# Kernel optimization log

Measured on AMD Instinct MI355X. Metric: run time of the kernel, lower is better.

Reference implementation:

```python
import jax, jax.numpy as jnp
import numpy as np

B, S, D = 2, 2048, 1024
H, DH = 16, 64  # num_head, head_dim; H*DH == D


def setup_inputs() -> dict:
    key = jax.random.key(0)
    ks = jax.random.split(key, 10)
    stdv = 1.0 / np.sqrt(D)
    def lin(k):
        kw, kb = jax.random.split(k)
        W = jax.random.uniform(kw, (D, D), jnp.float32, -stdv, stdv)
        b = jax.random.uniform(kb, (D,), jnp.float32, -stdv, stdv)
        return W, b
    Wq, bq = lin(ks[0]); Wk, bk = lin(ks[1]); Wv, bv = lin(ks[2]); Wo, bo = lin(ks[3])
    x = jax.random.normal(ks[4], (B, S, D), jnp.float32)
    # causal mask: True = attend
    mask = jnp.tril(jnp.ones((S, S), jnp.bool_))
    mask = jnp.broadcast_to(mask, (B, S, S))
    return {"x": x, "mask": mask, "Wq": Wq, "bq": bq, "Wk": Wk, "bk": bk,
            "Wv": Wv, "bv": bv, "Wo": Wo, "bo": bo}


def _split_head(t):
    # [B,S,D] -> [B*H, S, DH]
    return t.reshape(B, S, H, DH).transpose(0, 2, 1, 3).reshape(B * H, S, DH)


def _concat_head(t):
    # [B*H, S, DH] -> [B, S, D]
    return t.reshape(B, H, S, DH).transpose(0, 2, 1, 3).reshape(B, S, D)


def reference(x, mask, Wq, bq, Wk, bk, Wv, bv, Wo, bo):
    q = _split_head(x @ Wq.T + bq)
    k = _split_head(x @ Wk.T + bk)
    v = _split_head(x @ Wv.T + bv)
    scale = 1.0 / jnp.sqrt(jnp.float32(DH))
    # scores: [B, H, S, S], masked softmax (flash-attention math, unfused ref)
    scores = jnp.einsum('nqd,nkd->nqk', q, k).reshape(B, H, S, S) * scale
    scores = jnp.where(mask[:, None, :, :], scores, jnp.finfo(scores.dtype).min)
    attn = jax.nn.softmax(scores, axis=-1)
    out = jnp.einsum('bhqk,nkd->bhqd', attn, v.reshape(B, H, S, DH).reshape(B * H, S, DH)).reshape(B * H, S, DH) if False else jnp.einsum('nqk,nkd->nqd', attn.reshape(B * H, S, S), v)
    return _concat_head(out) @ Wo.T + bo
```

## Files before the change

### kernel.cpp

```cpp
#include <hip/hip_runtime.h>
#include <cstdint>

#define S_LEN  2048
#define NH     16
#define DHEAD  64
#define DMODEL 1024

typedef __bf16 bf16x8 __attribute__((ext_vector_type(8)));
typedef __bf16 bf16x2 __attribute__((ext_vector_type(2)));
typedef float  f32x4  __attribute__((ext_vector_type(4)));

__device__ __forceinline__ unsigned short f2bf(float x) {
  union { float f; unsigned int u; } c; c.f = x;
  unsigned int u = c.u;
  return (unsigned short)((u + 0x7fffu + ((u >> 16) & 1u)) >> 16);
}

__device__ __forceinline__ unsigned int pkbf(float a, float b) {
#if __has_builtin(__builtin_amdgcn_cvt_pk_bf16_f32)
  bf16x2 r = __builtin_amdgcn_cvt_pk_bf16_f32(a, b);
  return *(unsigned int*)&r;
#else
  return (unsigned int)f2bf(a) | ((unsigned int)f2bf(b) << 16);
#endif
}

__device__ __forceinline__ unsigned short f2bf1(float x) {
#if __has_builtin(__builtin_amdgcn_cvt_pk_bf16_f32)
  bf16x2 r = __builtin_amdgcn_cvt_pk_bf16_f32(x, x);
  union { bf16x2 v; unsigned int u; } c; c.v = r;
  return (unsigned short)(c.u & 0xffffu);
#else
  return f2bf(x);
#endif
}

__device__ __forceinline__ __bf16 us2bf(unsigned short u) {
  union { unsigned short u; __bf16 b; } c; c.u = u; return c.b;
}

__device__ __forceinline__ void glds16(const void* g, void* l) {
  __builtin_amdgcn_global_load_lds(
      (const __attribute__((address_space(1))) void*)g,
      (__attribute__((address_space(3))) void*)l, 16, 0, 0);
}

__device__ __forceinline__ f32x4 mfma16(bf16x8 a, bf16x8 b, f32x4 c) {
  return __builtin_amdgcn_mfma_f32_16x16x32_bf16(a, b, c, 0, 0, 0);
}

__global__ void cvt_all(const float* __restrict__ x,
                        const float* __restrict__ Wq,
                        const float* __restrict__ Wk,
                        const float* __restrict__ Wv,
                        const float* __restrict__ Wo,
                        unsigned short* __restrict__ xb,
                        unsigned short* __restrict__ wqkv,
                        unsigned short* __restrict__ wo) {
  const int b = blockIdx.x;
  const float* src;
  unsigned short* dst;
  int off;
  if (b < 4096)      { src = x;  dst = xb;                off = b; }
  else if (b < 5120) { src = Wq; dst = wqkv;              off = b - 4096; }
  else if (b < 6144) { src = Wk; dst = wqkv + (1 << 20);  off = b - 5120; }
  else if (b < 7168) { src = Wv; dst = wqkv + (2 << 20);  off = b - 6144; }
  else               { src = Wo; dst = wo;                off = b - 7168; }
  const int i = (off * 256 + threadIdx.x) * 4;
  float4 v = *(const float4*)&src[i];
  uint2 r;
  r.x = pkbf(v.x, v.y);
  r.y = pkbf(v.z, v.w);
  *(uint2*)&dst[i] = r;
}

template<int MODE, int BN>
__global__ __launch_bounds__(256)
void gemm_bt(const unsigned short* __restrict__ A,
             const unsigned short* __restrict__ W,
             const float* __restrict__ bias0,
             const float* __restrict__ bias1,
             const float* __restrict__ bias2,
             unsigned short* __restrict__ Qt,
             unsigned short* __restrict__ Kb,
             unsigned short* __restrict__ Vt,
             float* __restrict__ Out,
             int K) {
  constexpr int JN = BN / 32;
  __shared__ __align__(16) unsigned short As[2][128 * 32];
  __shared__ __align__(16) unsigned short Bs[2][BN * 32];
  const int t    = threadIdx.x;
  const int lane = t & 63;
  const int w    = t >> 6;
  const int lr   = lane & 15, lq = lane >> 4;
  const int wm   = (w >> 1) * 64, wn = (w & 1) * (BN / 2);
  const int m0   = blockIdx.y * 128, n0 = blockIdx.x * BN;
  const int ra   = t >> 2, ca = (t & 3) * 8;

  f32x4 acc[4][JN] = {};

  const int niter = K >> 6;
  for (int kk = 0; kk < niter; ++kk) {
    const int k0 = kk << 6;
#pragma unroll
    for (int kh = 0; kh < 2; ++kh) {
      const int kc = k0 + kh * 32;
      glds16(A + (m0 + ra) * K + kc + ca,      &As[kh][ra * 32 + ca]);
      glds16(A + (m0 + 64 + ra) * K + kc + ca, &As[kh][(64 + ra) * 32 + ca]);
      glds16(W + (n0 + ra) * K + kc + ca,      &Bs[kh][ra * 32 + ca]);
      if (BN == 128)
        glds16(W + (n0 + 64 + ra) * K + kc + ca, &Bs[kh][(64 + ra) * 32 + ca]);
    }
    __syncthreads();
#pragma unroll
    for (int kh = 0; kh < 2; ++kh) {
      bf16x8 af[4], bg[JN];
#pragma unroll
      for (int i = 0; i < 4; ++i)
        af[i] = *(const bf16x8*)&As[kh][(wm + i * 16 + lr) * 32 + lq * 8];
#pragma unroll
      for (int j = 0; j < JN; ++j)
        bg[j] = *(const bf16x8*)&Bs[kh][(wn + j * 16 + lr) * 32 + lq * 8];
#pragma unroll
      for (int i = 0; i < 4; ++i)
#pragma unroll
        for (int j = 0; j < JN; ++j)
          acc[i][j] = mfma16(af[i], bg[j], acc[i][j]);
    }
    __syncthreads();
  }

  if (MODE == 0) {
    const int tsel = n0 >> 10;
#pragma unroll
    for (int i = 0; i < 4; ++i) {
#pragma unroll
      for (int j = 0; j < JN; ++j) {
        const int mb = m0 + wm + i * 16 + lq * 4;
        const int n  = n0 + wn + j * 16 + lr;
        const int d  = n & 1023;
        const int bidx = mb >> 11, s = mb & (S_LEN - 1);
        const int h = d >> 6, dh = d & 63;
        const int bh = bidx * NH + h;
        const float bv0 = (tsel == 0) ? bias0[d] : ((tsel == 1) ? bias1[d] : bias2[d]);
        if (tsel == 0) {
          const float sc = 0.125f * 1.44269504088896f;
          uint2 pv;
          pv.x = pkbf((acc[i][j][0] + bv0) * sc, (acc[i][j][1] + bv0) * sc);
          pv.y = pkbf((acc[i][j][2] + bv0) * sc, (acc[i][j][3] + bv0) * sc);
          *(uint2*)&Qt[(bh * DHEAD + dh) * S_LEN + s] = pv;
        } else if (tsel == 2) {
          uint2 pv;
          pv.x = pkbf(acc[i][j][0] + bv0, acc[i][j][1] + bv0);
          pv.y = pkbf(acc[i][j][2] + bv0, acc[i][j][3] + bv0);
          *(uint2*)&Vt[(bh * DHEAD + dh) * S_LEN + s] = pv;
        } else {
#pragma unroll
          for (int r = 0; r < 4; ++r)
            Kb[(bh * S_LEN + s + r) * DHEAD + dh] = f2bf1(acc[i][j][r] + bv0);
        }
      }
    }
  } else {
#pragma unroll
    for (int i = 0; i < 4; ++i)
#pragma unroll
      for (int j = 0; j < JN; ++j)
#pragma unroll
        for (int r = 0; r < 4; ++r) {
          const int m = m0 + wm + i * 16 + lq * 4 + r;
          const int n = n0 + wn + j * 16 + lr;
          Out[m * DMODEL + n] = acc[i][j][r] + bias0[n];
        }
  }
}

__global__ __launch_bounds__(256, 2)
void flash_kernel(const unsigned short* __restrict__ Qt,
                  const unsigned short* __restrict__ Kb,
                  const unsigned short* __restrict__ Vt,
                  unsigned short* __restrict__ Ocat) {
  __shared__ __align__(16) unsigned short Ks[2][2][64 * 32];
  __shared__ __align__(16) unsigned short Vs[2][2][64 * 32];
  __shared__ __align__(16) unsigned short pls[4][1024];
  const int w = threadIdx.x >> 6, lane = threadIdx.x & 63;
  const int lr = lane & 15, lq = lane >> 4;
  const int bh = blockIdx.x;
  const int pp = blockIdx.y;
  const char* Kc = (const char*)(Kb + bh * (S_LEN * DHEAD));
  const char* Vc = (const char*)(Vt + bh * (DHEAD * S_LEN));
  const unsigned short* Qp = Qt + bh * (DHEAD * S_LEN);
  const int bb = bh >> 4, h = bh & 15;
  unsigned short* pw = &pls[w][0];
  const int swz = lr & 7;

  const int hh  = w & 1;
  const int rbb = (w >> 1) * 2;
  const int rlane = lane >> 2;
  const int slane = lane & 3;
  const int swslot = (slane ^ ((rlane >> 1) & 3)) * 16;
  const int rsw = (lq ^ ((lr >> 1) & 3)) * 8;

  bf16x8 ones;
#pragma unroll
  for (int j = 0; j < 8; ++j) ones[j] = (__bf16)1.0f;

  auto run_strip = [&](int sb) {
    const int nfull = sb;
    const int q0 = sb * 64 + w * 16;
    bf16x8 qlo, qhi;
#pragma unroll
    for (int j = 0; j < 8; ++j) {
      qlo[j] = us2bf(Qp[(lq * 8 + j) * S_LEN + q0 + lr]);
      qhi[j] = us2bf(Qp[(32 + lq * 8 + j) * S_LEN + q0 + lr]);
    }
    f32x4 o[4] = {};
    f32x4 lacc = {};

    auto stage = [&](int buf, int kt) {
      const int sk0 = kt << 6;
#pragma unroll
      for (int j = 0; j < 2; ++j) {
        const int rb = rbb + j;
        glds16(Kc + (sk0 + rb * 16 + rlane) * 128 + hh * 64 + swslot,
               &Ks[buf][hh][rb * 16 * 32]);
        glds16(Vc + (rb * 16 + rlane) * 4096 + (sk0 + hh * 32) * 2 + swslot,
               &Vs[buf][hh][rb * 16 * 32]);
      }
    };

    stage(0, 0);
    for (int kt = 0; kt <= nfull; ++kt) {
      const int buf = kt & 1;
      __syncthreads();
      if (kt < nfull) stage(1 - buf, kt + 1);

      f32x4 st[4] = {};
      const unsigned short* Kl = Ks[buf][0];
      const unsigned short* Kh = Ks[buf][1];
#pragma unroll
      for (int t = 0; t < 4; ++t) {
        st[t] = mfma16(*(const bf16x8*)&Kl[(t * 16 + lr) * 32 + rsw], qlo, st[t]);
        st[t] = mfma16(*(const bf16x8*)&Kh[(t * 16 + lr) * 32 + rsw], qhi, st[t]);
      }
      float p[4][4];
#pragma unroll
      for (int t = 0; t < 4; ++t)
#pragma unroll
        for (int r = 0; r < 4; ++r)
          p[t][r] = __builtin_amdgcn_exp2f(st[t][r]);
      if (kt == nfull) {
        const int q = q0 + lr, sk0 = kt << 6;
#pragma unroll
        for (int t = 0; t < 4; ++t)
#pragma unroll
          for (int r = 0; r < 4; ++r) {
            const int k = sk0 + t * 16 + lq * 4 + r;
            if (k > q) p[t][r] = 0.f;
          }
      }

#pragma unroll
      for (int t = 0; t < 4; ++t) {
        uint2 pk;
        pk.x = pkbf(p[t][0], p[t][1]);
        pk.y = pkbf(p[t][2], p[t][3]);
        const int g = t * 2 + (lq >> 1);
        *(uint2*)&pw[lr * 64 + ((g ^ swz) << 3) + ((lq & 1) << 2)] = pk;
      }
      const bf16x8 pf0 = *(const bf16x8*)&pw[lr * 64 + ((lq ^ swz) << 3)];
      const bf16x8 pf1 = *(const bf16x8*)&pw[lr * 64 + (((4 + lq) ^ swz) << 3)];
      const unsigned short* Vl = Vs[buf][0];
      const unsigned short* Vh = Vs[buf][1];
#pragma unroll
      for (int tt = 0; tt < 4; ++tt) {
        o[tt] = mfma16(*(const bf16x8*)&Vl[(tt * 16 + lr) * 32 + rsw], pf0, o[tt]);
        o[tt] = mfma16(*(const bf16x8*)&Vh[(tt * 16 + lr) * 32 + rsw], pf1, o[tt]);
      }
      lacc = mfma16(ones, pf0, lacc);
      lacc = mfma16(ones, pf1, lacc);
    }

    const float inv = 1.f / lacc[0];
#pragma unroll
    for (int tt = 0; tt < 4; ++tt) {
      uint2 ov;
      ov.x = pkbf(o[tt][0] * inv, o[tt][1] * inv);
      ov.y = pkbf(o[tt][2] * inv, o[tt][3] * inv);
      *(uint2*)&Ocat[(bb * S_LEN + q0 + lr) * DMODEL + h * DHEAD + tt * 16 + lq * 4] = ov;
    }
    __syncthreads();
  };

  run_strip(31 - pp);
  run_strip(pp);
}

extern "C" void kernel_launch(void* const* d_in, const int* in_sizes, int n_in,
                              void* d_out, int out_size, void* d_ws, size_t ws_size,
                              hipStream_t stream) {
  const float* x  = (const float*)d_in[0];
  const float* Wq = (const float*)d_in[2];
  const float* bq = (const float*)d_in[3];
  const float* Wk = (const float*)d_in[4];
  const float* bk = (const float*)d_in[5];
  const float* Wv = (const float*)d_in[6];
  const float* bv = (const float*)d_in[7];
  const float* Wo = (const float*)d_in[8];
  const float* bo = (const float*)d_in[9];
  float* out = (float*)d_out;

  char* ws = (char*)d_ws;
  unsigned short* xb   = (unsigned short*)(ws);
  unsigned short* wqkv = (unsigned short*)(ws + (8ull  << 20));
  unsigned short* wo   = (unsigned short*)(ws + (14ull << 20));
  unsigned short* Qt   = (unsigned short*)(ws + (16ull << 20));
  unsigned short* Kb   = (unsigned short*)(ws + (24ull << 20));
  unsigned short* Vt   = (unsigned short*)(ws + (32ull << 20));
  unsigned short* Ocat = (unsigned short*)(ws + (40ull << 20));

  cvt_all<<<8192, 256, 0, stream>>>(x, Wq, Wk, Wv, Wo, xb, wqkv, wo);

  gemm_bt<0, 128><<<dim3(24, 32), 256, 0, stream>>>(xb, wqkv, bq, bk, bv,
                                                    Qt, Kb, Vt, nullptr, 1024);
  flash_kernel<<<dim3(32, 16), 256, 0, stream>>>(Qt, Kb, Vt, Ocat);
  gemm_bt<1, 64><<<dim3(16, 32), 256, 0, stream>>>(Ocat, wo, bo, nullptr, nullptr,
                                                   nullptr, nullptr, nullptr, out, 1024);
}
```

Measured before the change: 201.4 us.

## Rewrite flash attention with 32x32 MFMA, split-K waves and permlane P reuse

Moves the flash kernel from 16x16x32 to 32x32x16 bf16 MFMA. Each wave now owns 32 query rows and handles alternate 64-key tiles, so two waves split the key range and their partial O and row sums are merged through LDS at the end. The P operand is rearranged with permlane32_swap instead of a round trip through LDS, and Q is now stored row-major so each lane loads it as a vector. This adds swizzled 64-wide K/V staging, an LDS reduction step and more registers per wave, which may lower occupancy.

```diff
diff --git a/kernel.cpp b/kernel.cpp
--- a/kernel.cpp
+++ b/kernel.cpp
@@ -9,6 +9,7 @@
 typedef __bf16 bf16x8 __attribute__((ext_vector_type(8)));
 typedef __bf16 bf16x2 __attribute__((ext_vector_type(2)));
 typedef float  f32x4  __attribute__((ext_vector_type(4)));
+typedef float  f32x16 __attribute__((ext_vector_type(16)));
 
 __device__ __forceinline__ unsigned short f2bf(float x) {
   union { float f; unsigned int u; } c; c.f = x;
@@ -47,6 +48,20 @@
 
 __device__ __forceinline__ f32x4 mfma16(bf16x8 a, bf16x8 b, f32x4 c) {
   return __builtin_amdgcn_mfma_f32_16x16x32_bf16(a, b, c, 0, 0, 0);
+}
+
+__device__ __forceinline__ f32x16 mfma32(bf16x8 a, bf16x8 b, f32x16 c) {
+  return __builtin_amdgcn_mfma_f32_32x32x16_bf16(a, b, c, 0, 0, 0);
+}
+
+__device__ __forceinline__ void plswap(unsigned int &a, unsigned int &b) {
+#if __has_builtin(__builtin_amdgcn_permlane32_swap)
+  typedef unsigned int uint2v __attribute__((ext_vector_type(2)));
+  uint2v r = __builtin_amdgcn_permlane32_swap(a, b, false, false);
+  a = r[0]; b = r[1];
+#else
+  asm("v_permlane32_swap_b32 %0, %1" : "+v"(a), "+v"(b));
+#endif
 }
 
 __global__ void cvt_all(const float* __restrict__ x,
@@ -145,10 +160,9 @@
         const float bv0 = (tsel == 0) ? bias0[d] : ((tsel == 1) ? bias1[d] : bias2[d]);
         if (tsel == 0) {
           const float sc = 0.125f * 1.44269504088896f;
-          uint2 pv;
-          pv.x = pkbf((acc[i][j][0] + bv0) * sc, (acc[i][j][1] + bv0) * sc);
-          pv.y = pkbf((acc[i][j][2] + bv0) * sc, (acc[i][j][3] + bv0) * sc);
-          *(uint2*)&Qt[(bh * DHEAD + dh) * S_LEN + s] = pv;
+#pragma unroll
+          for (int r = 0; r < 4; ++r)
+            Qt[(bh * S_LEN + s + r) * DHEAD + dh] = f2bf1((acc[i][j][r] + bv0) * sc);
         } else if (tsel == 2) {
           uint2 pv;
           pv.x = pkbf(acc[i][j][0] + bv0, acc[i][j][1] + bv0);
@@ -180,114 +194,139 @@
                   const unsigned short* __restrict__ Kb,
                   const unsigned short* __restrict__ Vt,
                   unsigned short* __restrict__ Ocat) {
-  __shared__ __align__(16) unsigned short Ks[2][2][64 * 32];
-  __shared__ __align__(16) unsigned short Vs[2][2][64 * 32];
-  __shared__ __align__(16) unsigned short pls[4][1024];
+  __shared__ __align__(16) unsigned short Ks[2][2][64 * 64];
+  __shared__ __align__(16) unsigned short Vs[2][2][64 * 64];
+  __shared__ float MlS[2][32];
   const int w = threadIdx.x >> 6, lane = threadIdx.x & 63;
-  const int lr = lane & 15, lq = lane >> 4;
+  const int l31 = lane & 31, half = lane >> 5;
+  const int qh = w & 1, sub = w >> 1;
   const int bh = blockIdx.x;
   const int pp = blockIdx.y;
   const char* Kc = (const char*)(Kb + bh * (S_LEN * DHEAD));
   const char* Vc = (const char*)(Vt + bh * (DHEAD * S_LEN));
-  const unsigned short* Qp = Qt + bh * (DHEAD * S_LEN);
-  const int bb = bh >> 4, h = bh & 15;
-  unsigned short* pw = &pls[w][0];
-  const int swz = lr & 7;
-
-  const int hh  = w & 1;
-  const int rbb = (w >> 1) * 2;
-  const int rlane = lane >> 2;
-  const int slane = lane & 3;
-  const int swslot = (slane ^ ((rlane >> 1) & 3)) * 16;
-  const int rsw = (lq ^ ((lr >> 1) & 3)) * 8;
+  const unsigned short* Qp = Qt + bh * (S_LEN * DHEAD);
+  const int bb = bh >> 4, hd = bh & 15;
 
   bf16x8 ones;
 #pragma unroll
   for (int j = 0; j < 8; ++j) ones[j] = (__bf16)1.0f;
 
   auto run_strip = [&](int sb) {
-    const int nfull = sb;
-    const int q0 = sb * 64 + w * 16;
-    bf16x8 qlo, qhi;
-#pragma unroll
-    for (int j = 0; j < 8; ++j) {
-      qlo[j] = us2bf(Qp[(lq * 8 + j) * S_LEN + q0 + lr]);
-      qhi[j] = us2bf(Qp[(32 + lq * 8 + j) * S_LEN + q0 + lr]);
-    }
-    f32x4 o[4] = {};
-    f32x4 lacc = {};
-
-    auto stage = [&](int buf, int kt) {
-      const int sk0 = kt << 6;
-#pragma unroll
-      for (int j = 0; j < 2; ++j) {
-        const int rb = rbb + j;
-        glds16(Kc + (sk0 + rb * 16 + rlane) * 128 + hh * 64 + swslot,
-               &Ks[buf][hh][rb * 16 * 32]);
-        glds16(Vc + (rb * 16 + rlane) * 4096 + (sk0 + hh * 32) * 2 + swslot,
-               &Vs[buf][hh][rb * 16 * 32]);
+    const int len = sb + 1;
+    const int nit = (len + 1) >> 1;
+    const int q0 = sb * 64;
+    const int qa = q0 + qh * 32 + l31;
+    bf16x8 qf[4];
+#pragma unroll
+    for (int d = 0; d < 4; ++d)
+      qf[d] = *(const bf16x8*)&Qp[qa * 64 + d * 16 + half * 8];
+    f32x16 o0 = {}, o1 = {}, lacc = {};
+
+    auto stage = [&](int buf, int it) {
+#pragma unroll
+      for (int s2 = 0; s2 < 2; ++s2) {
+        const int kt = 2 * it + s2;
+#pragma unroll
+        for (int h8 = 0; h8 < 2; ++h8) {
+          const int rb = w * 16 + h8 * 8;
+          const int r  = rb + (lane >> 3);
+          const int gs = (lane & 7) ^ (r & 7) ^ ((r >> 3) & 3);
+          glds16(Kc + (kt * 64 + r) * 128 + gs * 16, &Ks[buf][s2][rb * 64]);
+          glds16(Vc + r * 4096 + kt * 128 + gs * 16, &Vs[buf][s2][rb * 64]);
+        }
       }
     };
 
     stage(0, 0);
-    for (int kt = 0; kt <= nfull; ++kt) {
-      const int buf = kt & 1;
+    for (int it = 0; it < nit; ++it) {
+      const int buf = it & 1;
       __syncthreads();
-      if (kt < nfull) stage(1 - buf, kt + 1);
-
-      f32x4 st[4] = {};
-      const unsigned short* Kl = Ks[buf][0];
-      const unsigned short* Kh = Ks[buf][1];
-#pragma unroll
-      for (int t = 0; t < 4; ++t) {
-        st[t] = mfma16(*(const bf16x8*)&Kl[(t * 16 + lr) * 32 + rsw], qlo, st[t]);
-        st[t] = mfma16(*(const bf16x8*)&Kh[(t * 16 + lr) * 32 + rsw], qhi, st[t]);
-      }
-      float p[4][4];
-#pragma unroll
-      for (int t = 0; t < 4; ++t)
-#pragma unroll
-        for (int r = 0; r < 4; ++r)
-          p[t][r] = __builtin_amdgcn_exp2f(st[t][r]);
-      if (kt == nfull) {
-        const int q = q0 + lr, sk0 = kt << 6;
-#pragma unroll
-        for (int t = 0; t < 4; ++t)
-#pragma unroll
-          for (int r = 0; r < 4; ++r) {
-            const int k = sk0 + t * 16 + lq * 4 + r;
-            if (k > q) p[t][r] = 0.f;
+      if (it + 1 < nit) stage(1 - buf, it + 1);
+      const int kt = 2 * it + sub;
+      if (kt < len) {
+        const unsigned short* Kt = &Ks[buf][sub][0];
+        const unsigned short* Vl = &Vs[buf][sub][0];
+        const int r0 = l31, r1 = 32 + l31;
+        const int x0 = (r0 & 7) ^ ((r0 >> 3) & 3);
+        const int x1 = (r1 & 7) ^ ((r1 >> 3) & 3);
+        f32x16 st0 = {}, st1 = {};
+#pragma unroll
+        for (int d = 0; d < 4; ++d) {
+          const int sl = d * 2 + half;
+          st0 = mfma32(*(const bf16x8*)&Kt[r0 * 64 + ((sl ^ x0) << 3)], qf[d], st0);
+          st1 = mfma32(*(const bf16x8*)&Kt[r1 * 64 + ((sl ^ x1) << 3)], qf[d], st1);
+        }
+        const bool diag = (kt == sb);
+        unsigned int pk0[8], pk1[8];
+#pragma unroll
+        for (int m = 0; m < 8; ++m) {
+          const int rA = 2 * m, rB = 2 * m + 1;
+          const int kA = (rA & 3) + 8 * (rA >> 2) + 4 * half;
+          const int kB = (rB & 3) + 8 * (rB >> 2) + 4 * half;
+          float e0 = __builtin_amdgcn_exp2f(st0[rA]);
+          float e1 = __builtin_amdgcn_exp2f(st0[rB]);
+          float f0 = __builtin_amdgcn_exp2f(st1[rA]);
+          float f1 = __builtin_amdgcn_exp2f(st1[rB]);
+          if (diag) {
+            e0 = (kt * 64 + kA > qa) ? 0.f : e0;
+            e1 = (kt * 64 + kB > qa) ? 0.f : e1;
+            f0 = (kt * 64 + 32 + kA > qa) ? 0.f : f0;
+            f1 = (kt * 64 + 32 + kB > qa) ? 0.f : f1;
           }
-      }
-
-#pragma unroll
-      for (int t = 0; t < 4; ++t) {
-        uint2 pk;
-        pk.x = pkbf(p[t][0], p[t][1]);
-        pk.y = pkbf(p[t][2], p[t][3]);
-        const int g = t * 2 + (lq >> 1);
-        *(uint2*)&pw[lr * 64 + ((g ^ swz) << 3) + ((lq & 1) << 2)] = pk;
-      }
-      const bf16x8 pf0 = *(const bf16x8*)&pw[lr * 64 + ((lq ^ swz) << 3)];
-      const bf16x8 pf1 = *(const bf16x8*)&pw[lr * 64 + (((4 + lq) ^ swz) << 3)];
-      const unsigned short* Vl = Vs[buf][0];
-      const unsigned short* Vh = Vs[buf][1];
-#pragma unroll
-      for (int tt = 0; tt < 4; ++tt) {
-        o[tt] = mfma16(*(const bf16x8*)&Vl[(tt * 16 + lr) * 32 + rsw], pf0, o[tt]);
-        o[tt] = mfma16(*(const bf16x8*)&Vh[(tt * 16 + lr) * 32 + rsw], pf1, o[tt]);
-      }
-      lacc = mfma16(ones, pf0, lacc);
-      lacc = mfma16(ones, pf1, lacc);
-    }
-
-    const float inv = 1.f / lacc[0];
-#pragma unroll
-    for (int tt = 0; tt < 4; ++tt) {
-      uint2 ov;
-      ov.x = pkbf(o[tt][0] * inv, o[tt][1] * inv);
-      ov.y = pkbf(o[tt][2] * inv, o[tt][3] * inv);
-      *(uint2*)&Ocat[(bb * S_LEN + q0 + lr) * DMODEL + h * DHEAD + tt * 16 + lq * 4] = ov;
+          pk0[m] = pkbf(e0, e1);
+          pk1[m] = pkbf(f0, f1);
+        }
+#pragma unroll
+        for (int s = 0; s < 4; ++s) {
+          unsigned int u, u2, v, v2;
+          if (s == 0)      { u = pk0[0]; u2 = pk0[1]; v = pk0[2]; v2 = pk0[3]; }
+          else if (s == 1) { u = pk0[4]; u2 = pk0[5]; v = pk0[6]; v2 = pk0[7]; }
+          else if (s == 2) { u = pk1[0]; u2 = pk1[1]; v = pk1[2]; v2 = pk1[3]; }
+          else             { u = pk1[4]; u2 = pk1[5]; v = pk1[6]; v2 = pk1[7]; }
+          plswap(u, v);
+          plswap(u2, v2);
+          union { unsigned int ui[4]; bf16x8 bv; } pf;
+          pf.ui[0] = u; pf.ui[1] = u2; pf.ui[2] = v; pf.ui[3] = v2;
+          const int sl = s * 2 + half;
+          o0 = mfma32(*(const bf16x8*)&Vl[r0 * 64 + ((sl ^ x0) << 3)], pf.bv, o0);
+          o1 = mfma32(*(const bf16x8*)&Vl[r1 * 64 + ((sl ^ x1) << 3)], pf.bv, o1);
+          lacc = mfma32(ones, pf.bv, lacc);
+        }
+      }
+    }
+
+    float* Mo = (float*)&Ks[1 - ((nit - 1) & 1)][0][0];
+    const int qrow = qh * 32 + l31;
+    if (sub == 1) {
+      if (lane < 32) MlS[qh][l31] = lacc[0];
+#pragma unroll
+      for (int g = 0; g < 4; ++g) {
+        const int sl0 = 2 * g + half;
+        const int sl1 = 8 + 2 * g + half;
+        f32x4 s0 = { o0[4 * g], o0[4 * g + 1], o0[4 * g + 2], o0[4 * g + 3] };
+        f32x4 s1 = { o1[4 * g], o1[4 * g + 1], o1[4 * g + 2], o1[4 * g + 3] };
+        *(f32x4*)&Mo[qrow * 64 + ((sl0 ^ (qrow & 15)) << 2)] = s0;
+        *(f32x4*)&Mo[qrow * 64 + ((sl1 ^ (qrow & 15)) << 2)] = s1;
+      }
+    }
+    __syncthreads();
+    if (sub == 0) {
+      const float inv = 1.f / (lacc[0] + MlS[qh][l31]);
+      unsigned short* Or = Ocat + (bb * S_LEN + q0 + qrow) * DMODEL + hd * DHEAD;
+#pragma unroll
+      for (int g = 0; g < 4; ++g) {
+        const int sl0 = 2 * g + half;
+        const int sl1 = 8 + 2 * g + half;
+        const f32x4 m0 = *(const f32x4*)&Mo[qrow * 64 + ((sl0 ^ (qrow & 15)) << 2)];
+        const f32x4 m1 = *(const f32x4*)&Mo[qrow * 64 + ((sl1 ^ (qrow & 15)) << 2)];
+        uint2 ov0, ov1;
+        ov0.x = pkbf((o0[4 * g]     + m0[0]) * inv, (o0[4 * g + 1] + m0[1]) * inv);
+        ov0.y = pkbf((o0[4 * g + 2] + m0[2]) * inv, (o0[4 * g + 3] + m0[3]) * inv);
+        ov1.x = pkbf((o1[4 * g]     + m1[0]) * inv, (o1[4 * g + 1] + m1[1]) * inv);
+        ov1.y = pkbf((o1[4 * g + 2] + m1[2]) * inv, (o1[4 * g + 3] + m1[3]) * inv);
+        *(uint2*)&Or[8 * g + 4 * half]      = ov0;
+        *(uint2*)&Or[32 + 8 * g + 4 * half] = ov1;
+      }
     }
     __syncthreads();
   };
```

New measurement: 194.4 us. 1.04x faster.
